# Kernel optimization log

Measured on AMD Instinct MI355X. Metric: run time of the kernel, lower is better.

Reference implementation:

```python
import jax, jax.numpy as jnp
import numpy as np

NEG_SLOPE = 0.2
EPS = 1e-12


def _spmm(edge_row, edge_col, edge_w, h, n):
    # out[i] = sum_{e: row=i} w_e * h[col_e]   (row-normalized adjacency @ h)
    msgs = edge_w[:, None] * h[edge_col]
    return jax.ops.segment_sum(msgs, edge_row, num_segments=n)


def setup_inputs() -> dict:
    key = jax.random.key(0)
    ks = jax.random.split(key, 6)
    n, e, c_in, c_hid, c_out = 50000, 1600000, 300, 2048, 2048
    x = jax.random.normal(ks[0], (n, c_in), dtype=jnp.float32)
    # xavier-uniform-like init
    W1 = jax.random.uniform(ks[1], (c_in, c_hid), jnp.float32, -1.0, 1.0) * np.sqrt(6.0 / (c_in + c_hid))
    b1 = jnp.zeros((c_hid,), jnp.float32)
    W2 = jax.random.uniform(ks[2], (c_hid, c_out), jnp.float32, -1.0, 1.0) * np.sqrt(6.0 / (c_hid + c_out))
    b2 = jnp.zeros((c_out,), jnp.float32)
    edge_row = jax.random.randint(ks[3], (e,), 0, n, dtype=jnp.int32)
    edge_col = jax.random.randint(ks[4], (e,), 0, n, dtype=jnp.int32)
    return {"x": x, "W1": W1, "b1": b1, "W2": W2, "b2": b2,
            "edge_row": edge_row, "edge_col": edge_col}


def reference(x, W1, b1, W2, b2, edge_row, edge_col):
    n = x.shape[0]
    # 'in' normalization of unit-weight adjacency: w_e = 1 / in_degree(row_e)
    deg = jax.ops.segment_sum(jnp.ones_like(edge_row, dtype=jnp.float32), edge_row, num_segments=n)
    edge_w = 1.0 / jnp.maximum(deg, 1.0)
    edge_w = edge_w[edge_row]
    # layer 1: adj @ (x @ W1) + b1, LeakyReLU(0.2)  (dropout is identity in eval)
    h = _spmm(edge_row, edge_col, edge_w, x @ W1, n) + b1
    h = jnp.where(h >= 0, h, NEG_SLOPE * h)
    # last layer: no relu
    h = _spmm(edge_row, edge_col, edge_w, h @ W2, n) + b2
    # F.normalize: row-wise L2 with eps clamp
    norm = jnp.maximum(jnp.sqrt(jnp.sum(h * h, axis=-1, keepdims=True)), EPS)
    return h / norm
```

## Files before the change

### kernel.cpp

```cpp
#include <hip/hip_runtime.h>
#include <math.h>

typedef unsigned short ushort_t;
using bf16x8  = __attribute__((ext_vector_type(8))) short;
using f32x4   = __attribute__((ext_vector_type(4))) float;
using ushort8 = __attribute__((ext_vector_type(8))) unsigned short;

__device__ __forceinline__ unsigned short f2bf(float f) {
    union { float f; unsigned int u; } v; v.f = f;
    unsigned int r = v.u + 0x7FFFu + ((v.u >> 16) & 1u);
    return (unsigned short)(r >> 16);
}
__device__ __forceinline__ float bf2f(unsigned short u) {
    union { unsigned int u; float f; } v; v.u = ((unsigned int)u) << 16;
    return v.f;
}

#if defined(__has_builtin)
#if __has_builtin(__builtin_amdgcn_cvt_f32_fp8) && __has_builtin(__builtin_amdgcn_cvt_pk_fp8_f32)
#define FP8_HW 1
#endif
#endif

__device__ __forceinline__ unsigned char f2fp8(float v) {
#ifdef FP8_HW
    unsigned int p = __builtin_amdgcn_cvt_pk_fp8_f32(v, v, 0, false);
    return (unsigned char)(p & 0xFFu);
#else
    union { float f; unsigned u; } b; b.f = v;
    unsigned s = (b.u >> 24) & 0x80u;
    float a = fabsf(v);
    if (a >= 448.f) return (unsigned char)(s | 0x7E);
    if (a < 0.015625f) {
        int m = (int)rintf(a * 512.0f);
        if (m >= 8) return (unsigned char)(s | 0x08);
        return (unsigned char)(s | (unsigned)m);
    }
    unsigned u = b.u & 0x7FFFFFFFu;
    u += 0x7FFFFu + ((u >> 20) & 1u);
    int e8 = (int)((u >> 23) & 0xFF) - 120;
    unsigned M = (u >> 20) & 7u;
    if (e8 > 15 || (e8 == 15 && M == 7u)) return (unsigned char)(s | 0x7E);
    return (unsigned char)(s | ((unsigned)e8 << 3) | M);
#endif
}

#ifdef FP8_HW
#define ACC8(ac, w) do { \
    ac[0] += __builtin_amdgcn_cvt_f32_fp8((int)(w).x, 0); \
    ac[1] += __builtin_amdgcn_cvt_f32_fp8((int)(w).x, 1); \
    ac[2] += __builtin_amdgcn_cvt_f32_fp8((int)(w).x, 2); \
    ac[3] += __builtin_amdgcn_cvt_f32_fp8((int)(w).x, 3); \
    ac[4] += __builtin_amdgcn_cvt_f32_fp8((int)(w).y, 0); \
    ac[5] += __builtin_amdgcn_cvt_f32_fp8((int)(w).y, 1); \
    ac[6] += __builtin_amdgcn_cvt_f32_fp8((int)(w).y, 2); \
    ac[7] += __builtin_amdgcn_cvt_f32_fp8((int)(w).y, 3); \
} while (0)
#else
__device__ __forceinline__ float fp82f(unsigned u) {
    unsigned s = u >> 7, e = (u >> 3) & 15u, m = u & 7u;
    union { unsigned u; float f; } nb;
    nb.u = (s << 31) | ((e + 120u) << 23) | (m << 20);
    float sub = (float)(int)m * 0.001953125f;
    sub = s ? -sub : sub;
    return e ? nb.f : sub;
}
#define ACC8(ac, w) do { \
    ac[0] += fp82f(((w).x      ) & 0xFFu); \
    ac[1] += fp82f(((w).x >>  8) & 0xFFu); \
    ac[2] += fp82f(((w).x >> 16) & 0xFFu); \
    ac[3] += fp82f(((w).x >> 24)        ); \
    ac[4] += fp82f(((w).y      ) & 0xFFu); \
    ac[5] += fp82f(((w).y >>  8) & 0xFFu); \
    ac[6] += fp82f(((w).y >> 16) & 0xFFu); \
    ac[7] += fp82f(((w).y >> 24)        ); \
} while (0)
#endif

typedef const __attribute__((address_space(1))) void* gas_ptr;
typedef __attribute__((address_space(3))) void* las_ptr;
__device__ __forceinline__ void gload16(const void* g, void* l) {
    __builtin_amdgcn_global_load_lds((gas_ptr)g, (las_ptr)l, 16, 0, 0);
}


__global__ void k_zero_i32(int* __restrict__ p, int n) {
    int i = blockIdx.x * blockDim.x + threadIdx.x;
    if (i < n) p[i] = 0;
}

__global__ void k_count_deg(const int* __restrict__ erow, int* __restrict__ deg, int e) {
    for (int i = blockIdx.x * blockDim.x + threadIdx.x; i < e; i += gridDim.x * blockDim.x)
        atomicAdd(&deg[erow[i]], 1);
}

__global__ __launch_bounds__(1024) void k_scan(const int* __restrict__ deg, int* __restrict__ ptr,
                                               int* __restrict__ cursor, int n) {
    __shared__ int buf[1024];
    __shared__ int carry_s;
    int t = threadIdx.x;
    if (t == 0) { carry_s = 0; ptr[0] = 0; }
    __syncthreads();
    for (int base = 0; base < n; base += 1024) {
        int i = base + t;
        int v = (i < n) ? deg[i] : 0;
        buf[t] = v;
        __syncthreads();
        #pragma unroll
        for (int off = 1; off < 1024; off <<= 1) {
            int xv = (t >= off) ? buf[t - off] : 0;
            __syncthreads();
            buf[t] += xv;
            __syncthreads();
        }
        int carry = carry_s;
        int incl = buf[t] + carry;
        if (i < n) { ptr[i + 1] = incl; cursor[i] = incl - v; }
        int bsum = buf[1023];
        __syncthreads();
        if (t == 0) carry_s = carry + bsum;
        __syncthreads();
    }
}

__global__ void k_scatter(const int* __restrict__ erow, const int* __restrict__ ecol,
                          int* __restrict__ cursor, int* __restrict__ csr_col, int e) {
    for (int i = blockIdx.x * blockDim.x + threadIdx.x; i < e; i += gridDim.x * blockDim.x) {
        int pos = atomicAdd(&cursor[erow[i]], 1);
        csr_col[pos] = ecol[i];
    }
}


__global__ __launch_bounds__(256) void k_cvt_wT(const float* __restrict__ W, unsigned short* __restrict__ WT,
                                                int K, int N, int Kpad) {
    __shared__ float tile[32][33];
    int kp0 = blockIdx.x * 32, n0 = blockIdx.y * 32;
    int tx = threadIdx.x & 31, ty = threadIdx.x >> 5;
    #pragma unroll
    for (int ii = 0; ii < 4; ++ii) {
        int k = kp0 + ty + ii * 8;
        tile[ty + ii * 8][tx] = (k < K) ? W[(size_t)k * N + n0 + tx] : 0.0f;
    }
    __syncthreads();
    #pragma unroll
    for (int ii = 0; ii < 4; ++ii) {
        int n = n0 + ty + ii * 8;
        WT[(size_t)n * Kpad + kp0 + tx] = f2bf(tile[tx][ty + ii * 8]);
    }
}


__global__ __launch_bounds__(128) void k_spmm1(const int* __restrict__ ptr, const int* __restrict__ col,
                                               const float* __restrict__ x, unsigned short* __restrict__ ax) {
    int r = blockIdx.x;
    int t = threadIdx.x;
    int s = ptr[r], e = ptr[r + 1];
    bool act = t < 75;
    const float4* xb = (const float4*)x;
    float4 a0 = {0.f, 0.f, 0.f, 0.f}, a1 = {0.f, 0.f, 0.f, 0.f};
    int p = s;
    for (; p + 1 < e; p += 2) {
        int c0 = col[p], c1 = col[p + 1];
        if (act) {
            float4 v0 = xb[(size_t)c0 * 75 + t];
            float4 v1 = xb[(size_t)c1 * 75 + t];
            a0.x += v0.x; a0.y += v0.y; a0.z += v0.z; a0.w += v0.w;
            a1.x += v1.x; a1.y += v1.y; a1.z += v1.z; a1.w += v1.w;
        }
    }
    if (p < e && act) {
        float4 v = xb[(size_t)col[p] * 75 + t];
        a0.x += v.x; a0.y += v.y; a0.z += v.z; a0.w += v.w;
    }
    float w = 1.0f / fmaxf((float)(e - s), 1.0f);
    unsigned short* o = ax + (size_t)r * 320;
    if (act) {
        ushort4 ov;
        ov.x = f2bf((a0.x + a1.x) * w);
        ov.y = f2bf((a0.y + a1.y) * w);
        ov.z = f2bf((a0.z + a1.z) * w);
        ov.w = f2bf((a0.w + a1.w) * w);
        *(ushort4*)(o + t * 4) = ov;
    } else if (t < 80) {
        ushort4 z = {0, 0, 0, 0};
        *(ushort4*)(o + t * 4) = z;
    }
}


template <int EPI>
__global__ __launch_bounds__(256) void k_mfma_gemm(const unsigned short* __restrict__ A, int lda,
                                                   const unsigned short* __restrict__ BT, int ldb,
                                                   const float* __restrict__ bias,
                                                   void* __restrict__ Cv,
                                                   int M, int N, int K) {
    __shared__ __align__(16) unsigned short As[128 * 32];
    __shared__ __align__(16) unsigned short Bs[128 * 32];
    int tid = threadIdx.x;
    int lane = tid & 63;
    int wid = tid >> 6;
    int wm = wid >> 1, wn = wid & 1;
    int bm = blockIdx.y * 128, bn = blockIdx.x * 128;

    f32x4 zero4 = {0.f, 0.f, 0.f, 0.f};
    f32x4 acc[4][4];
    #pragma unroll
    for (int i = 0; i < 4; ++i)
        #pragma unroll
        for (int j = 0; j < 4; ++j) acc[i][j] = zero4;

    int srow = tid >> 2;
    int scol = (tid & 3) * 8;
    int ar0 = bm + srow;      if (ar0 >= M) ar0 = M - 1;
    int ar1 = bm + srow + 64; if (ar1 >= M) ar1 = M - 1;
    const unsigned short* gA0 = A + (size_t)ar0 * lda + scol;
    const unsigned short* gA1 = A + (size_t)ar1 * lda + scol;
    const unsigned short* gB0 = BT + (size_t)(bn + srow) * ldb + scol;
    const unsigned short* gB1 = BT + (size_t)(bn + srow + 64) * ldb + scol;

    int kq = (lane >> 4) * 8;
    int rsel = lane & 15;

    for (int k0 = 0; k0 < K; k0 += 32) {
        gload16(gA0 + k0, &As[(size_t)tid * 8]);
        gload16(gA1 + k0, &As[(size_t)(tid + 256) * 8]);
        gload16(gB0 + k0, &Bs[(size_t)tid * 8]);
        gload16(gB1 + k0, &Bs[(size_t)(tid + 256) * 8]);
        __syncthreads();

        bf16x8 af[4], bfr[4];
        #pragma unroll
        for (int i = 0; i < 4; ++i) {
            af[i]  = *(const bf16x8*)&As[(wm * 64 + i * 16 + rsel) * 32 + kq];
            bfr[i] = *(const bf16x8*)&Bs[(wn * 64 + i * 16 + rsel) * 32 + kq];
        }
        #pragma unroll
        for (int i = 0; i < 4; ++i)
            #pragma unroll
            for (int j = 0; j < 4; ++j)
                acc[i][j] = __builtin_amdgcn_mfma_f32_16x16x32_bf16(af[i], bfr[j], acc[i][j], 0, 0, 0);
        __syncthreads();
    }

    #pragma unroll
    for (int i = 0; i < 4; ++i) {
        int row_base = bm + wm * 64 + i * 16 + (lane >> 4) * 4;
        #pragma unroll
        for (int j = 0; j < 4; ++j) {
            int colg = bn + wn * 64 + j * 16 + (lane & 15);
            float bv = (EPI == 1) ? bias[colg] : 0.0f;
            #pragma unroll
            for (int r = 0; r < 4; ++r) {
                int row = row_base + r;
                if (row < M) {
                    float v = acc[i][j][r];
                    if (EPI == 1) {
                        v += bv; v = (v >= 0.f) ? v : 0.2f * v;
                        ((unsigned short*)Cv)[(size_t)row * N + colg] = f2bf(v);
                    } else {
                        ((unsigned char*)Cv)[(size_t)row * N + colg] = f2fp8(v * 32.0f);
                    }
                }
            }
        }
    }
}


__global__ __launch_bounds__(512) void k_gemm8p_fp8(const unsigned short* __restrict__ A, int lda,
                                                    const unsigned short* __restrict__ BT, int ldb,
                                                    unsigned char* __restrict__ C,
                                                    int M, int N, int K) {
    __shared__ __align__(16) unsigned short As_l[2][2][8192];
    __shared__ __align__(16) unsigned short Bs_l[2][2][8192];

    const int tid  = threadIdx.x;
    const int lane = tid & 63;
    const int wid  = tid >> 6;
    const int wm   = wid >> 2;
    const int wn   = wid & 3;
    const int bm = blockIdx.y * 256, bn = blockIdx.x * 256;

    int rA[2], rB[2], cc[2], ldst[2];
    #pragma unroll
    for (int i = 0; i < 2; ++i) {
        int P = wid * 2048 + i * 1024 + lane * 16;
        int L = P ^ (((P >> 7) & 3) << 4);
        int r = L >> 6;
        cc[i] = (L & 63) >> 1;
        int ra = bm + r; if (ra >= M) ra = M - 1;
        rA[i] = ra;
        rB[i] = bn + r;
        ldst[i] = P >> 1;
    }

    const int rsel = lane & 15, kq8 = (lane >> 4) * 8;
    int aoff[8], boff[4];
    #pragma unroll
    for (int fi = 0; fi < 8; ++fi) {
        int row = wm * 128 + fi * 16 + rsel;
        aoff[fi] = row * 32 + (kq8 ^ (((row >> 1) & 3) << 3));
    }
    #pragma unroll
    for (int fj = 0; fj < 4; ++fj) {
        int row = wn * 64 + fj * 16 + rsel;
        boff[fj] = row * 32 + (kq8 ^ (((row >> 1) & 3) << 3));
    }

    f32x4 acc[8][4];
    #pragma unroll
    for (int fi = 0; fi < 8; ++fi)
        #pragma unroll
        for (int fj = 0; fj < 4; ++fj) { f32x4 z = {0.f,0.f,0.f,0.f}; acc[fi][fj] = z; }

    #define STAGE_K(buf, h, k0) do { \
        gload16(A  + (size_t)rA[0] * lda + (k0) + (h) * 32 + cc[0], &As_l[buf][h][ldst[0]]); \
        gload16(A  + (size_t)rA[1] * lda + (k0) + (h) * 32 + cc[1], &As_l[buf][h][ldst[1]]); \
        gload16(BT + (size_t)rB[0] * ldb + (k0) + (h) * 32 + cc[0], &Bs_l[buf][h][ldst[0]]); \
        gload16(BT + (size_t)rB[1] * ldb + (k0) + (h) * 32 + cc[1], &Bs_l[buf][h][ldst[1]]); \
    } while (0)

    const int NT = K / 64;

    STAGE_K(0, 0, 0);
    STAGE_K(0, 1, 0);
    asm volatile("s_waitcnt vmcnt(4)\n\ts_barrier" ::: "memory");

    for (int t = 0; t < NT; ++t) {
        const int bt = t & 1;
        const int kn = (t + 1) * 64;
        const bool pf = (t + 1 < NT);
        #pragma unroll
        for (int ph = 0; ph < 2; ++ph) {
            if (pf) STAGE_K(bt ^ 1, ph, kn);
            bf16x8 af[8], bfv[4];
            #pragma unroll
            for (int fi = 0; fi < 8; ++fi) af[fi] = *(const bf16x8*)&As_l[bt][ph][aoff[fi]];
            #pragma unroll
            for (int fj = 0; fj < 4; ++fj) bfv[fj] = *(const bf16x8*)&Bs_l[bt][ph][boff[fj]];
            __builtin_amdgcn_s_setprio(1);
            #pragma unroll
            for (int fi = 0; fi < 8; ++fi)
                #pragma unroll
                for (int fj = 0; fj < 4; ++fj)
                    acc[fi][fj] = __builtin_amdgcn_mfma_f32_16x16x32_bf16(af[fi], bfv[fj], acc[fi][fj], 0, 0, 0);
            __builtin_amdgcn_s_setprio(0);
            if (pf)                 asm volatile("s_waitcnt vmcnt(4)\n\ts_barrier" ::: "memory");
            else if (ph == 0)       asm volatile("s_waitcnt vmcnt(0)\n\ts_barrier" ::: "memory");
        }
    }
    #undef STAGE_K

    #pragma unroll
    for (int fi = 0; fi < 8; ++fi) {
        int row_base = bm + wm * 128 + fi * 16 + (lane >> 4) * 4;
        #pragma unroll
        for (int fj = 0; fj < 4; ++fj) {
            int colg = bn + wn * 64 + fj * 16 + (lane & 15);
            #pragma unroll
            for (int r = 0; r < 4; ++r) {
                int row = row_base + r;
                if (row < M) C[(size_t)row * N + colg] = f2fp8(acc[fi][fj][r] * 32.0f);
            }
        }
    }
}


__global__ __launch_bounds__(256) void k_spmm2_norm(const int* __restrict__ ptr, const int* __restrict__ col,
                                                    const unsigned char* __restrict__ H2,
                                                    const float* __restrict__ b2,
                                                    float* __restrict__ out) {
    const int C = 2048;
    int r = blockIdx.x, t = threadIdx.x;
    int s = ptr[r], e = ptr[r + 1];
    float ac0[8] = {}, ac1[8] = {}, ac2[8] = {}, ac3[8] = {};
    const uint2* base = (const uint2*)(H2 + t * 8);
    int p = s;
    for (; p + 3 < e; p += 4) {
        uint2 w0 = base[(size_t)col[p]     * 256];
        uint2 w1 = base[(size_t)col[p + 1] * 256];
        uint2 w2 = base[(size_t)col[p + 2] * 256];
        uint2 w3 = base[(size_t)col[p + 3] * 256];
        ACC8(ac0, w0); ACC8(ac1, w1); ACC8(ac2, w2); ACC8(ac3, w3);
    }
    for (; p < e; ++p) {
        uint2 w = base[(size_t)col[p] * 256];
        ACC8(ac0, w);
    }
    float w = 1.0f / (32.0f * fmaxf((float)(e - s), 1.0f));
    float ss = 0.f;
    float vv[8];
    #pragma unroll
    for (int j = 0; j < 8; ++j) {
        float v = (ac0[j] + ac1[j] + ac2[j] + ac3[j]) * w + b2[t * 8 + j];
        vv[j] = v;
        ss += v * v;
    }
    __shared__ float red[4];
    __shared__ float scale_s;
    #pragma unroll
    for (int off = 32; off > 0; off >>= 1) ss += __shfl_down(ss, off, 64);
    int lane = t & 63, wid = t >> 6;
    if (lane == 0) red[wid] = ss;
    __syncthreads();
    if (t == 0) {
        float tot = red[0] + red[1] + red[2] + red[3];
        scale_s = 1.0f / fmaxf(sqrtf(tot), 1e-12f);
    }
    __syncthreads();
    float sc = scale_s;
    float* o = out + (size_t)r * C + t * 8;
    float4 o0 = {vv[0] * sc, vv[1] * sc, vv[2] * sc, vv[3] * sc};
    float4 o1 = {vv[4] * sc, vv[5] * sc, vv[6] * sc, vv[7] * sc};
    *(float4*)o = o0;
    *(float4*)(o + 4) = o1;
}


extern "C" void kernel_launch(void* const* d_in, const int* in_sizes, int n_in,
                              void* d_out, int out_size, void* d_ws, size_t ws_size,
                              hipStream_t stream) {
    const float* x  = (const float*)d_in[0];
    const float* W1 = (const float*)d_in[1];
    const float* b1 = (const float*)d_in[2];
    const float* W2 = (const float*)d_in[3];
    const float* b2 = (const float*)d_in[4];
    const int* erow = (const int*)d_in[5];
    const int* ecol = (const int*)d_in[6];

    const int chid = in_sizes[2];
    const int cout = in_sizes[4];
    const int cin  = in_sizes[1] / chid;
    const int n    = in_sizes[0] / cin;
    const int e    = in_sizes[5];
    const int cinp = (cin + 31) & ~31;

    char* ws = (char*)d_ws;
    size_t off = 0;
    auto alloc = [&](size_t bytes) -> void* {
        void* p = ws + off;
        off += (bytes + 255) & ~(size_t)255;
        return p;
    };
    int*            deg     = (int*)alloc((size_t)n * 4);
    int*            ptr     = (int*)alloc((size_t)(n + 1) * 4);
    int*            cursor  = (int*)alloc((size_t)n * 4);
    int*            csr_col = (int*)alloc((size_t)e * 4);
    unsigned short* ax      = (unsigned short*)alloc((size_t)n * cinp * 2);
    unsigned short* W1T     = (unsigned short*)alloc((size_t)chid * cinp * 2);
    unsigned short* W2T     = (unsigned short*)alloc((size_t)cout * chid * 2);
    unsigned char*  H2f8    = (unsigned char*)alloc((size_t)n * cout);
    unsigned short* H1      = (unsigned short*)d_out;

    k_zero_i32<<<(n + 255) / 256, 256, 0, stream>>>(deg, n);
    k_count_deg<<<2048, 256, 0, stream>>>(erow, deg, e);
    k_scan<<<1, 1024, 0, stream>>>(deg, ptr, cursor, n);
    k_scatter<<<2048, 256, 0, stream>>>(erow, ecol, cursor, csr_col, e);

    dim3 gw1(cinp / 32, chid / 32);
    k_cvt_wT<<<gw1, 256, 0, stream>>>(W1, W1T, cin, chid, cinp);
    dim3 gw2(chid / 32, cout / 32);
    k_cvt_wT<<<gw2, 256, 0, stream>>>(W2, W2T, chid, cout, chid);

    k_spmm1<<<n, 128, 0, stream>>>(ptr, csr_col, x, ax);

    dim3 g1(chid / 128, (n + 127) / 128);
    k_mfma_gemm<1><<<g1, 256, 0, stream>>>(ax, cinp, W1T, cinp, b1, (void*)H1, n, chid, cinp);

    dim3 g2(cout / 256, (n + 255) / 256);
    k_gemm8p_fp8<<<g2, 512, 0, stream>>>(H1, chid, W2T, chid, H2f8, n, cout, chid);

    k_spmm2_norm<<<n, 256, 0, stream>>>(ptr, csr_col, H2f8, b2, (float*)d_out);
}
```

Before: 1.855 ms.

## Use 4-slot K=32 LDS ring in fp8 GEMM and XCD-aware tile remap

The 256x256 GEMM's double-buffered K=64 stages become a 4-slot ring of K=32 slices with prefetch two steps ahead. Loads are split across the two MFMA halves and A fragments are loaded in halves to cut register pressure. Both GEMM kernels also remap block indices so consecutive tiles land on the same XCD, aiming for better L2 reuse. The risks are more barriers per K step and a waitcnt scheme that must still match the new outstanding-load counts.

```diff
diff --git a/kernel.cpp b/kernel.cpp
--- a/kernel.cpp
+++ b/kernel.cpp
@@ -83,6 +83,19 @@
     __builtin_amdgcn_global_load_lds((gas_ptr)g, (las_ptr)l, 16, 0, 0);
 }
 
+__device__ __forceinline__ void xcd_tile(int* col, int* row) {
+    int nx = gridDim.x;
+    int nwg = nx * gridDim.y;
+    int i = blockIdx.y * nx + blockIdx.x;
+    int l = i;
+    if ((nwg & 7) == 0) {
+        int cpx = nwg >> 3;
+        l = (i & 7) * cpx + (i >> 3);
+    }
+    *col = l % nx;
+    *row = l / nx;
+}
+
 
 __global__ void k_zero_i32(int* __restrict__ p, int n) {
     int i = blockIdx.x * blockDim.x + threadIdx.x;
@@ -201,7 +214,9 @@
     int lane = tid & 63;
     int wid = tid >> 6;
     int wm = wid >> 1, wn = wid & 1;
-    int bm = blockIdx.y * 128, bn = blockIdx.x * 128;
+    int tcol, trow;
+    xcd_tile(&tcol, &trow);
+    int bm = trow * 128, bn = tcol * 128;
 
     f32x4 zero4 = {0.f, 0.f, 0.f, 0.f};
     f32x4 acc[4][4];
@@ -272,15 +287,17 @@
                                                     const unsigned short* __restrict__ BT, int ldb,
                                                     unsigned char* __restrict__ C,
                                                     int M, int N, int K) {
-    __shared__ __align__(16) unsigned short As_l[2][2][8192];
-    __shared__ __align__(16) unsigned short Bs_l[2][2][8192];
+    __shared__ __align__(16) unsigned short As_l[4][8192];
+    __shared__ __align__(16) unsigned short Bs_l[4][8192];
 
     const int tid  = threadIdx.x;
     const int lane = tid & 63;
     const int wid  = tid >> 6;
     const int wm   = wid >> 2;
     const int wn   = wid & 3;
-    const int bm = blockIdx.y * 256, bn = blockIdx.x * 256;
+    int tcol, trow;
+    xcd_tile(&tcol, &trow);
+    const int bm = trow * 256, bn = tcol * 256;
 
     int rA[2], rB[2], cc[2], ldst[2];
     #pragma unroll
@@ -314,43 +331,54 @@
         #pragma unroll
         for (int fj = 0; fj < 4; ++fj) { f32x4 z = {0.f,0.f,0.f,0.f}; acc[fi][fj] = z; }
 
-    #define STAGE_K(buf, h, k0) do { \
-        gload16(A  + (size_t)rA[0] * lda + (k0) + (h) * 32 + cc[0], &As_l[buf][h][ldst[0]]); \
-        gload16(A  + (size_t)rA[1] * lda + (k0) + (h) * 32 + cc[1], &As_l[buf][h][ldst[1]]); \
-        gload16(BT + (size_t)rB[0] * ldb + (k0) + (h) * 32 + cc[0], &Bs_l[buf][h][ldst[0]]); \
-        gload16(BT + (size_t)rB[1] * ldb + (k0) + (h) * 32 + cc[1], &Bs_l[buf][h][ldst[1]]); \
+    #define STAGE_P(b, k0, i) do { \
+        gload16(A  + (size_t)rA[i] * lda + (k0) + cc[i], &As_l[b][ldst[i]]); \
+        gload16(BT + (size_t)rB[i] * ldb + (k0) + cc[i], &Bs_l[b][ldst[i]]); \
     } while (0)
 
-    const int NT = K / 64;
-
-    STAGE_K(0, 0, 0);
-    STAGE_K(0, 1, 0);
+    const int NT = K / 32;
+
+    STAGE_P(0, 0, 0);  STAGE_P(0, 0, 1);
+    STAGE_P(1, 32, 0); STAGE_P(1, 32, 1);
     asm volatile("s_waitcnt vmcnt(4)\n\ts_barrier" ::: "memory");
 
     for (int t = 0; t < NT; ++t) {
-        const int bt = t & 1;
-        const int kn = (t + 1) * 64;
-        const bool pf = (t + 1 < NT);
-        #pragma unroll
-        for (int ph = 0; ph < 2; ++ph) {
-            if (pf) STAGE_K(bt ^ 1, ph, kn);
-            bf16x8 af[8], bfv[4];
-            #pragma unroll
-            for (int fi = 0; fi < 8; ++fi) af[fi] = *(const bf16x8*)&As_l[bt][ph][aoff[fi]];
-            #pragma unroll
-            for (int fj = 0; fj < 4; ++fj) bfv[fj] = *(const bf16x8*)&Bs_l[bt][ph][boff[fj]];
+        const int bt = t & 3;
+        const bool pf = (t + 2 < NT);
+        const int kn = (t + 2) * 32;
+        if (pf) STAGE_P((t + 2) & 3, kn, 0);
+        bf16x8 bfv[4];
+        #pragma unroll
+        for (int fj = 0; fj < 4; ++fj) bfv[fj] = *(const bf16x8*)&Bs_l[bt][boff[fj]];
+        {
+            bf16x8 af[4];
+            #pragma unroll
+            for (int fi = 0; fi < 4; ++fi) af[fi] = *(const bf16x8*)&As_l[bt][aoff[fi]];
             __builtin_amdgcn_s_setprio(1);
             #pragma unroll
-            for (int fi = 0; fi < 8; ++fi)
+            for (int fi = 0; fi < 4; ++fi)
                 #pragma unroll
                 for (int fj = 0; fj < 4; ++fj)
                     acc[fi][fj] = __builtin_amdgcn_mfma_f32_16x16x32_bf16(af[fi], bfv[fj], acc[fi][fj], 0, 0, 0);
             __builtin_amdgcn_s_setprio(0);
-            if (pf)                 asm volatile("s_waitcnt vmcnt(4)\n\ts_barrier" ::: "memory");
-            else if (ph == 0)       asm volatile("s_waitcnt vmcnt(0)\n\ts_barrier" ::: "memory");
-        }
-    }
-    #undef STAGE_K
+        }
+        if (pf) STAGE_P((t + 2) & 3, kn, 1);
+        {
+            bf16x8 af[4];
+            #pragma unroll
+            for (int fi = 0; fi < 4; ++fi) af[fi] = *(const bf16x8*)&As_l[bt][aoff[fi + 4]];
+            __builtin_amdgcn_s_setprio(1);
+            #pragma unroll
+            for (int fi = 0; fi < 4; ++fi)
+                #pragma unroll
+                for (int fj = 0; fj < 4; ++fj)
+                    acc[fi + 4][fj] = __builtin_amdgcn_mfma_f32_16x16x32_bf16(af[fi], bfv[fj], acc[fi + 4][fj], 0, 0, 0);
+            __builtin_amdgcn_s_setprio(0);
+        }
+        if (pf)                asm volatile("s_waitcnt vmcnt(4)\n\ts_barrier" ::: "memory");
+        else if (t + 2 == NT)  asm volatile("s_waitcnt vmcnt(0)\n\ts_barrier" ::: "memory");
+    }
+    #undef STAGE_P
 
     #pragma unroll
     for (int fi = 0; fi < 8; ++fi) {
```

Result: no change. 1.862 ms (+0.4%).
